# Kernel tuning notes

Measured on AMD Instinct MI355X. Metric: run time of the kernel, lower is better.

Reference implementation:

```python
import jax, jax.numpy as jnp
import numpy as np


def setup_inputs() -> dict:
    key = jax.random.key(0)
    B, U, I, H = 8192, 16, 128, 128
    k = jax.random.split(key, 6)
    s = 1.0 / np.sqrt(H)  # PyTorch GRU init scale (uniform(-s, s)); use scaled normal for test data
    return {
        "inputs": jax.random.normal(k[0], (B, U, I), dtype=jnp.float32),
        "hidden": jax.random.normal(k[1], (B, U, H), dtype=jnp.float32),
        "w_ih": jax.random.normal(k[2], (U, 3 * H, I), dtype=jnp.float32) * s,
        "w_hh": jax.random.normal(k[3], (U, 3 * H, H), dtype=jnp.float32) * s,
        "b_ih": jax.random.normal(k[4], (U, 3 * H), dtype=jnp.float32) * s,
        "b_hh": jax.random.normal(k[5], (U, 3 * H), dtype=jnp.float32) * s,
    }


def reference(inputs, hidden, w_ih, w_hh, b_ih, b_hh):
    # Grouped single-step GRU: one independent GRU cell per unit u, batched via einsum.
    # PyTorch GRU gate order in the 3H dim: [reset, update, new].
    H = hidden.shape[-1]
    # gates_x[b,u,g] = sum_i inputs[b,u,i] * w_ih[u,g,i] + b_ih[u,g]
    gx = jnp.einsum("bui,ugi->bug", inputs, w_ih) + b_ih  # (B, U, 3H)
    gh = jnp.einsum("buh,ugh->bug", hidden, w_hh) + b_hh  # (B, U, 3H)
    xr, xz, xn = gx[..., :H], gx[..., H:2 * H], gx[..., 2 * H:]
    hr, hz, hn = gh[..., :H], gh[..., H:2 * H], gh[..., 2 * H:]
    r = jax.nn.sigmoid(xr + hr)
    z = jax.nn.sigmoid(xz + hz)
    n = jnp.tanh(xn + r * hn)
    return (1.0 - z) * n + z * hidden  # (B, U, H)
```

## Files before the change

### kernel.cpp

```cpp
#include <hip/hip_runtime.h>
#include <hip/hip_bf16.h>

typedef __attribute__((ext_vector_type(8))) short  short8;
typedef __attribute__((ext_vector_type(4))) float  floatx4;

#define UH   2048
#define XPAD 264

#define MFMA16(a,b,c) __builtin_amdgcn_mfma_f32_16x16x32_bf16(a, b, c, 0, 0, 0)

static __device__ __forceinline__ unsigned int pkbf16(float a, float b) {
    __hip_bfloat162 p = __float22bfloat162_rn(make_float2(a, b));
    return *(unsigned int*)&p;
}

__global__ __launch_bounds__(256) void prep(const float* __restrict__ w_ih,
                                            const float* __restrict__ w_hh,
                                            const float* __restrict__ b_ih,
                                            const float* __restrict__ b_hh,
                                            __hip_bfloat16* __restrict__ Wc,
                                            float* __restrict__ bias_c) {
    if (blockIdx.x < 768) {
        int t   = blockIdx.x * 256 + threadIdx.x;
        int k8  = t & 31;
        int row = t >> 5;
        int u   = row / 384;
        int g   = row - u * 384;
        int k   = k8 * 8;
        const float* src = (k < 128) ? (w_ih + (size_t)row * 128 + k)
                                     : (w_hh + (size_t)row * 128 + (k - 128));
        float4 v0 = ((const float4*)src)[0];
        float4 v1 = ((const float4*)src)[1];
        uint4 w;
        w.x = pkbf16(v0.x, v0.y);
        w.y = pkbf16(v0.z, v0.w);
        w.z = pkbf16(v1.x, v1.y);
        w.w = pkbf16(v1.z, v1.w);
        int gt = g >> 4, lr = g & 15;
        int s  = k8 >> 2, lq = k8 & 3;
        size_t off = (size_t)((u * 24 + gt) * 8 + s) * 512 + (lq * 16 + lr) * 8;
        *(uint4*)(Wc + off) = w;
    } else {
        int idx = (blockIdx.x - 768) * 256 + threadIdx.x;
        int u = idx >> 9;
        int g = idx & 511;
        float v;
        if (g < 256)       v = b_ih[u * 384 + g] + b_hh[u * 384 + g];
        else if (g < 384)  v = b_ih[u * 384 + g];
        else               v = b_hh[u * 384 + (g - 128)];
        bias_c[idx] = v;
    }
}

__global__ __launch_bounds__(512, 2) void gru_fused(
    const float* __restrict__ inputs, const float* __restrict__ hidden,
    const __hip_bfloat16* __restrict__ Wc, const float* __restrict__ bias_c,
    float* __restrict__ out)
{
    __shared__ __align__(16) __hip_bfloat16 Xs[2][64][XPAD];

    const int bx   = blockIdx.x;
    const int u    = ((bx & 7) << 1) | ((bx >> 3) & 1);
    const int mt0  = (bx >> 4) * 8;
    const int tid  = threadIdx.x;
    const int lane = tid & 63;
    const int wv   = tid >> 6;
    const int lr   = lane & 15;
    const int lq   = lane >> 4;

    const short* WgU = (const short*)Wc + (size_t)u * 98304 + lane * 8;
    short8 fR[8], fZ[8], fN[8];
    #pragma unroll
    for (int s = 0; s < 8; ++s) {
        fR[s] = *(const short8*)(WgU + (size_t)(       wv * 8 + s) * 512);
        fZ[s] = *(const short8*)(WgU + (size_t)( 64 +  wv * 8 + s) * 512);
        fN[s] = *(const short8*)(WgU + (size_t)(128 +  wv * 8 + s) * 512);
    }

    const int   c   = wv * 16 + lr;
    const float br  = bias_c[u * 512 + c];
    const float bz  = bias_c[u * 512 + 128 + c];
    const float bxn = bias_c[u * 512 + 256 + c];
    const float bhn = bias_c[u * 512 + 384 + c];

    const int scol = (tid & 63) * 4;
    const float* sbase = ((scol < 128) ? (inputs + scol)
                                       : (hidden + (scol - 128)))
                       + (size_t)u * 128;

    float4 stg[8];

    auto ISSUE = [&](int mt) {
        const float* p = sbase + (size_t)(mt * 64 + wv) * UH;
        #pragma unroll
        for (int i = 0; i < 8; ++i)
            stg[i] = *(const float4*)(p + (size_t)(i * 8) * UH);
    };
    auto WRITE = [&](int buf) {
        #pragma unroll
        for (int i = 0; i < 8; ++i) {
            uint2 w;
            w.x = pkbf16(stg[i].x, stg[i].y);
            w.y = pkbf16(stg[i].z, stg[i].w);
            *(uint2*)&Xs[buf][i * 8 + wv][scol] = w;
        }
    };
    auto BARRIER = [&]() {
        asm volatile("s_waitcnt lgkmcnt(0)" ::: "memory");
        __builtin_amdgcn_sched_barrier(0);
        __builtin_amdgcn_s_barrier();
        __builtin_amdgcn_sched_barrier(0);
    };

    ISSUE(mt0 + 0);
    WRITE(0);
    ISSUE(mt0 + 1);
    BARRIER();

    #pragma unroll 1
    for (int j = 0; j < 8; ++j) {
        const int buf = j & 1;

        floatx4 aR[4], aZ[4], aXN[4], aHN[4];
        #pragma unroll
        for (int m4 = 0; m4 < 4; ++m4) {
            aR[m4]  = (floatx4){0.f, 0.f, 0.f, 0.f};
            aZ[m4]  = (floatx4){0.f, 0.f, 0.f, 0.f};
            aXN[m4] = (floatx4){0.f, 0.f, 0.f, 0.f};
            aHN[m4] = (floatx4){0.f, 0.f, 0.f, 0.f};
        }
        #pragma unroll
        for (int s = 0; s < 8; ++s) {
            short8 aF[4];
            #pragma unroll
            for (int m4 = 0; m4 < 4; ++m4)
                aF[m4] = *(const short8*)((const short*)&Xs[buf][m4 * 16 + lr][0]
                                          + s * 32 + lq * 8);
            #pragma unroll
            for (int m4 = 0; m4 < 4; ++m4) {
                aR[m4] = MFMA16(aF[m4], fR[s], aR[m4]);
                aZ[m4] = MFMA16(aF[m4], fZ[s], aZ[m4]);
                if (s < 4) aXN[m4] = MFMA16(aF[m4], fN[s], aXN[m4]);
                else       aHN[m4] = MFMA16(aF[m4], fN[s], aHN[m4]);
            }
        }

        float* obase = out + (size_t)(mt0 + j) * 64 * UH + u * 128 + c;
        #pragma unroll
        for (int m4 = 0; m4 < 4; ++m4) {
            #pragma unroll
            for (int r = 0; r < 4; ++r) {
                const int m = m4 * 16 + lq * 4 + r;
                float rv = __builtin_amdgcn_rcpf(1.f + __expf(-(aR[m4][r] + br)));
                float zv = __builtin_amdgcn_rcpf(1.f + __expf(-(aZ[m4][r] + bz)));
                float npre = (aXN[m4][r] + bxn) + rv * (aHN[m4][r] + bhn);
                float nv = 2.f * __builtin_amdgcn_rcpf(1.f + __expf(-2.f * npre)) - 1.f;
                float hv = __bfloat162float(Xs[buf][m][128 + c]);
                obase[(size_t)m * UH] = nv + zv * (hv - nv);
            }
        }

        if (j < 7) {
            WRITE(buf ^ 1);
            if (j < 6) ISSUE(mt0 + j + 2);
            BARRIER();
        }
    }
}


extern "C" void kernel_launch(void* const* d_in, const int* in_sizes, int n_in,
                              void* d_out, int out_size, void* d_ws, size_t ws_size,
                              hipStream_t stream) {
    const float* inputs = (const float*)d_in[0];
    const float* hidden = (const float*)d_in[1];
    const float* w_ih   = (const float*)d_in[2];
    const float* w_hh   = (const float*)d_in[3];
    const float* b_ih   = (const float*)d_in[4];
    const float* b_hh   = (const float*)d_in[5];
    float* out = (float*)d_out;

    __hip_bfloat16* Wc = (__hip_bfloat16*)d_ws;
    float* bias_c = (float*)((char*)d_ws + (size_t)16 * 384 * 256 * 2);

    prep<<<dim3(800), dim3(256), 0, stream>>>(w_ih, w_hh, b_ih, b_hh, Wc, bias_c);
    gru_fused<<<dim3(256), dim3(512), 0, stream>>>(inputs, hidden, Wc, bias_c, out);
}
```

Before: 200.3 us.

## Fuse weight conversion into GRU kernel and transpose MFMA for vectorized stores

Drops the separate prep kernel: each block loads fp32 weights directly, converts them to bf16 MFMA fragments in registers, and folds the biases into the accumulator initial values. The MFMA operand order is swapped so each lane holds four consecutive output columns, which allows float4 output stores and a vector read of h from LDS. The epilogue is moved after the next tile's LDS write and global issue, and the barrier is deferred to overlap it. This removes one launch and the workspace round trip. In exchange, each block redundantly converts its unit's weights, 16 blocks per unit.

```diff
diff --git a/kernel.cpp b/kernel.cpp
--- a/kernel.cpp
+++ b/kernel.cpp
@@ -13,48 +13,15 @@
     __hip_bfloat162 p = __float22bfloat162_rn(make_float2(a, b));
     return *(unsigned int*)&p;
 }
-
-__global__ __launch_bounds__(256) void prep(const float* __restrict__ w_ih,
-                                            const float* __restrict__ w_hh,
-                                            const float* __restrict__ b_ih,
-                                            const float* __restrict__ b_hh,
-                                            __hip_bfloat16* __restrict__ Wc,
-                                            float* __restrict__ bias_c) {
-    if (blockIdx.x < 768) {
-        int t   = blockIdx.x * 256 + threadIdx.x;
-        int k8  = t & 31;
-        int row = t >> 5;
-        int u   = row / 384;
-        int g   = row - u * 384;
-        int k   = k8 * 8;
-        const float* src = (k < 128) ? (w_ih + (size_t)row * 128 + k)
-                                     : (w_hh + (size_t)row * 128 + (k - 128));
-        float4 v0 = ((const float4*)src)[0];
-        float4 v1 = ((const float4*)src)[1];
-        uint4 w;
-        w.x = pkbf16(v0.x, v0.y);
-        w.y = pkbf16(v0.z, v0.w);
-        w.z = pkbf16(v1.x, v1.y);
-        w.w = pkbf16(v1.z, v1.w);
-        int gt = g >> 4, lr = g & 15;
-        int s  = k8 >> 2, lq = k8 & 3;
-        size_t off = (size_t)((u * 24 + gt) * 8 + s) * 512 + (lq * 16 + lr) * 8;
-        *(uint4*)(Wc + off) = w;
-    } else {
-        int idx = (blockIdx.x - 768) * 256 + threadIdx.x;
-        int u = idx >> 9;
-        int g = idx & 511;
-        float v;
-        if (g < 256)       v = b_ih[u * 384 + g] + b_hh[u * 384 + g];
-        else if (g < 384)  v = b_ih[u * 384 + g];
-        else               v = b_hh[u * 384 + (g - 128)];
-        bias_c[idx] = v;
-    }
+static __device__ __forceinline__ float bf2f(unsigned short h) {
+    unsigned int u = (unsigned int)h << 16;
+    return *(float*)&u;
 }
 
 __global__ __launch_bounds__(512, 2) void gru_fused(
     const float* __restrict__ inputs, const float* __restrict__ hidden,
-    const __hip_bfloat16* __restrict__ Wc, const float* __restrict__ bias_c,
+    const float* __restrict__ w_ih,   const float* __restrict__ w_hh,
+    const float* __restrict__ b_ih,   const float* __restrict__ b_hh,
     float* __restrict__ out)
 {
     __shared__ __align__(16) __hip_bfloat16 Xs[2][64][XPAD];
@@ -68,20 +35,40 @@
     const int lr   = lane & 15;
     const int lq   = lane >> 4;
 
-    const short* WgU = (const short*)Wc + (size_t)u * 98304 + lane * 8;
+    auto loadW = [&](int gt, int s) -> short8 {
+        const int row = gt * 16 + lr;
+        const int k0  = s * 32 + lq * 8;
+        const float* src = (k0 < 128)
+            ? (w_ih + (size_t)(u * 384 + row) * 128 + k0)
+            : (w_hh + (size_t)(u * 384 + row) * 128 + (k0 - 128));
+        float4 v0 = ((const float4*)src)[0];
+        float4 v1 = ((const float4*)src)[1];
+        union { uint4 q; short8 s8; } cvt;
+        cvt.q.x = pkbf16(v0.x, v0.y);
+        cvt.q.y = pkbf16(v0.z, v0.w);
+        cvt.q.z = pkbf16(v1.x, v1.y);
+        cvt.q.w = pkbf16(v1.z, v1.w);
+        return cvt.s8;
+    };
     short8 fR[8], fZ[8], fN[8];
     #pragma unroll
     for (int s = 0; s < 8; ++s) {
-        fR[s] = *(const short8*)(WgU + (size_t)(       wv * 8 + s) * 512);
-        fZ[s] = *(const short8*)(WgU + (size_t)( 64 +  wv * 8 + s) * 512);
-        fN[s] = *(const short8*)(WgU + (size_t)(128 +  wv * 8 + s) * 512);
+        fR[s] = loadW(     wv, s);
+        fZ[s] = loadW( 8 + wv, s);
+        fN[s] = loadW(16 + wv, s);
     }
 
-    const int   c   = wv * 16 + lr;
-    const float br  = bias_c[u * 512 + c];
-    const float bz  = bias_c[u * 512 + 128 + c];
-    const float bxn = bias_c[u * 512 + 256 + c];
-    const float bhn = bias_c[u * 512 + 384 + c];
+    const int c0 = wv * 16 + lq * 4;
+    float4 bi = *(const float4*)(b_ih + u * 384 +       c0);
+    float4 bh = *(const float4*)(b_hh + u * 384 +       c0);
+    float4 zi = *(const float4*)(b_ih + u * 384 + 128 + c0);
+    float4 zh = *(const float4*)(b_hh + u * 384 + 128 + c0);
+    float4 ni = *(const float4*)(b_ih + u * 384 + 256 + c0);
+    float4 nh = *(const float4*)(b_hh + u * 384 + 256 + c0);
+    const floatx4 accR0  = (floatx4){bi.x + bh.x, bi.y + bh.y, bi.z + bh.z, bi.w + bh.w};
+    const floatx4 accZ0  = (floatx4){zi.x + zh.x, zi.y + zh.y, zi.z + zh.z, zi.w + zh.w};
+    const floatx4 accXN0 = (floatx4){ni.x, ni.y, ni.z, ni.w};
+    const floatx4 accHN0 = (floatx4){nh.x, nh.y, nh.z, nh.w};
 
     const int scol = (tid & 63) * 4;
     const float* sbase = ((scol < 128) ? (inputs + scol)
@@ -113,6 +100,12 @@
     };
 
     ISSUE(mt0 + 0);
+    #pragma unroll
+    for (int s = 0; s < 8; ++s) {
+        asm volatile("" : "+v"(fR[s]));
+        asm volatile("" : "+v"(fZ[s]));
+        asm volatile("" : "+v"(fN[s]));
+    }
     WRITE(0);
     ISSUE(mt0 + 1);
     BARRIER();
@@ -124,47 +117,53 @@
         floatx4 aR[4], aZ[4], aXN[4], aHN[4];
         #pragma unroll
         for (int m4 = 0; m4 < 4; ++m4) {
-            aR[m4]  = (floatx4){0.f, 0.f, 0.f, 0.f};
-            aZ[m4]  = (floatx4){0.f, 0.f, 0.f, 0.f};
-            aXN[m4] = (floatx4){0.f, 0.f, 0.f, 0.f};
-            aHN[m4] = (floatx4){0.f, 0.f, 0.f, 0.f};
+            aR[m4]  = accR0;
+            aZ[m4]  = accZ0;
+            aXN[m4] = accXN0;
+            aHN[m4] = accHN0;
         }
         #pragma unroll
         for (int s = 0; s < 8; ++s) {
-            short8 aF[4];
+            short8 xF[4];
             #pragma unroll
             for (int m4 = 0; m4 < 4; ++m4)
-                aF[m4] = *(const short8*)((const short*)&Xs[buf][m4 * 16 + lr][0]
+                xF[m4] = *(const short8*)((const short*)&Xs[buf][m4 * 16 + lr][0]
                                           + s * 32 + lq * 8);
             #pragma unroll
             for (int m4 = 0; m4 < 4; ++m4) {
-                aR[m4] = MFMA16(aF[m4], fR[s], aR[m4]);
-                aZ[m4] = MFMA16(aF[m4], fZ[s], aZ[m4]);
-                if (s < 4) aXN[m4] = MFMA16(aF[m4], fN[s], aXN[m4]);
-                else       aHN[m4] = MFMA16(aF[m4], fN[s], aHN[m4]);
-            }
-        }
-
-        float* obase = out + (size_t)(mt0 + j) * 64 * UH + u * 128 + c;
-        #pragma unroll
-        for (int m4 = 0; m4 < 4; ++m4) {
-            #pragma unroll
-            for (int r = 0; r < 4; ++r) {
-                const int m = m4 * 16 + lq * 4 + r;
-                float rv = __builtin_amdgcn_rcpf(1.f + __expf(-(aR[m4][r] + br)));
-                float zv = __builtin_amdgcn_rcpf(1.f + __expf(-(aZ[m4][r] + bz)));
-                float npre = (aXN[m4][r] + bxn) + rv * (aHN[m4][r] + bhn);
-                float nv = 2.f * __builtin_amdgcn_rcpf(1.f + __expf(-2.f * npre)) - 1.f;
-                float hv = __bfloat162float(Xs[buf][m][128 + c]);
-                obase[(size_t)m * UH] = nv + zv * (hv - nv);
+                aR[m4] = MFMA16(fR[s], xF[m4], aR[m4]);
+                aZ[m4] = MFMA16(fZ[s], xF[m4], aZ[m4]);
+                if (s < 4) aXN[m4] = MFMA16(fN[s], xF[m4], aXN[m4]);
+                else       aHN[m4] = MFMA16(fN[s], xF[m4], aHN[m4]);
             }
         }
 
         if (j < 7) {
             WRITE(buf ^ 1);
             if (j < 6) ISSUE(mt0 + j + 2);
-            BARRIER();
         }
+
+        #pragma unroll
+        for (int m4 = 0; m4 < 4; ++m4) {
+            const int m = m4 * 16 + lr;
+            ushort4 hq = *(const ushort4*)&Xs[buf][m][128 + c0];
+            unsigned short hs[4] = {hq.x, hq.y, hq.z, hq.w};
+            float4 o;
+            float* op = (float*)&o;
+            #pragma unroll
+            for (int r = 0; r < 4; ++r) {
+                float rv = __builtin_amdgcn_rcpf(1.f + __expf(-aR[m4][r]));
+                float zv = __builtin_amdgcn_rcpf(1.f + __expf(-aZ[m4][r]));
+                float npre = aXN[m4][r] + rv * aHN[m4][r];
+                float nv = 2.f * __builtin_amdgcn_rcpf(1.f + __expf(-2.f * npre)) - 1.f;
+                float hv = bf2f(hs[r]);
+                op[r] = nv + zv * (hv - nv);
+            }
+            float* orow = out + (size_t)((mt0 + j) * 64 + m) * UH + u * 128 + c0;
+            *(float4*)orow = o;
+        }
+
+        if (j < 7) BARRIER();
     }
 }
 
@@ -180,9 +179,6 @@
     const float* b_hh   = (const float*)d_in[5];
     float* out = (float*)d_out;
 
-    __hip_bfloat16* Wc = (__hip_bfloat16*)d_ws;
-    float* bias_c = (float*)((char*)d_ws + (size_t)16 * 384 * 256 * 2);
-
-    prep<<<dim3(800), dim3(256), 0, stream>>>(w_ih, w_hh, b_ih, b_hh, Wc, bias_c);
-    gru_fused<<<dim3(256), dim3(512), 0, stream>>>(inputs, hidden, Wc, bias_c, out);
+    gru_fused<<<dim3(256), dim3(512), 0, stream>>>(inputs, hidden,
+                                                   w_ih, w_hh, b_ih, b_hh, out);
 }
```

After: 202.8 us. No clear change (+1.3%).

## Shrink batch tile, stream weights from global per step, swap MFMA operands for vector stores

Applied to the files above, without the earlier changes.

Each block now handles 128 batch rows in 32-row tiles instead of 512 in 64-row tiles, and the grid grows to 1024 blocks with launch bounds raised to 4 blocks per CU. Weight fragments are reloaded from global/L2 on every k-step instead of being held in registers. This frees registers for higher occupancy but adds repeated weight traffic. MFMA operands are swapped so each lane owns four contiguous output columns, which allows float4 stores and float4 fp32 hidden loads. Biases now initialize the accumulators, and the hidden term uses the exact fp32 value rather than the bf16 copy in LDS.

```diff
diff --git a/kernel.cpp b/kernel.cpp
--- a/kernel.cpp
+++ b/kernel.cpp
@@ -52,53 +52,43 @@
     }
 }
 
-__global__ __launch_bounds__(512, 2) void gru_fused(
+__global__ __launch_bounds__(512, 4) void gru_fused(
     const float* __restrict__ inputs, const float* __restrict__ hidden,
     const __hip_bfloat16* __restrict__ Wc, const float* __restrict__ bias_c,
     float* __restrict__ out)
 {
-    __shared__ __align__(16) __hip_bfloat16 Xs[2][64][XPAD];
+    __shared__ __align__(16) __hip_bfloat16 Xs[2][32][XPAD];
 
     const int bx   = blockIdx.x;
     const int u    = ((bx & 7) << 1) | ((bx >> 3) & 1);
-    const int mt0  = (bx >> 4) * 8;
+    const int r0   = (bx >> 4) * 128;
     const int tid  = threadIdx.x;
     const int lane = tid & 63;
     const int wv   = tid >> 6;
     const int lr   = lane & 15;
     const int lq   = lane >> 4;
 
-    const short* WgU = (const short*)Wc + (size_t)u * 98304 + lane * 8;
-    short8 fR[8], fZ[8], fN[8];
-    #pragma unroll
-    for (int s = 0; s < 8; ++s) {
-        fR[s] = *(const short8*)(WgU + (size_t)(       wv * 8 + s) * 512);
-        fZ[s] = *(const short8*)(WgU + (size_t)( 64 +  wv * 8 + s) * 512);
-        fN[s] = *(const short8*)(WgU + (size_t)(128 +  wv * 8 + s) * 512);
-    }
+    const int c0 = wv * 16 + lq * 4;
+    const floatx4 accR0  = *(const floatx4*)(bias_c + u * 512 +       c0);
+    const floatx4 accZ0  = *(const floatx4*)(bias_c + u * 512 + 128 + c0);
+    const floatx4 accXN0 = *(const floatx4*)(bias_c + u * 512 + 256 + c0);
+    const floatx4 accHN0 = *(const floatx4*)(bias_c + u * 512 + 384 + c0);
 
-    const int   c   = wv * 16 + lr;
-    const float br  = bias_c[u * 512 + c];
-    const float bz  = bias_c[u * 512 + 128 + c];
-    const float bxn = bias_c[u * 512 + 256 + c];
-    const float bhn = bias_c[u * 512 + 384 + c];
-
-    const int scol = (tid & 63) * 4;
+    const int scol = lane * 4;
     const float* sbase = ((scol < 128) ? (inputs + scol)
                                        : (hidden + (scol - 128)))
                        + (size_t)u * 128;
 
-    float4 stg[8];
+    float4 stg[4];
 
-    auto ISSUE = [&](int mt) {
-        const float* p = sbase + (size_t)(mt * 64 + wv) * UH;
+    auto ISSUE = [&](int rowbase) {
         #pragma unroll
-        for (int i = 0; i < 8; ++i)
-            stg[i] = *(const float4*)(p + (size_t)(i * 8) * UH);
+        for (int i = 0; i < 4; ++i)
+            stg[i] = *(const float4*)(sbase + (size_t)(rowbase + i * 8 + wv) * UH);
     };
     auto WRITE = [&](int buf) {
         #pragma unroll
-        for (int i = 0; i < 8; ++i) {
+        for (int i = 0; i < 4; ++i) {
             uint2 w;
             w.x = pkbf16(stg[i].x, stg[i].y);
             w.y = pkbf16(stg[i].z, stg[i].w);
@@ -112,58 +102,60 @@
         __builtin_amdgcn_sched_barrier(0);
     };
 
-    ISSUE(mt0 + 0);
+    const short* WgU = (const short*)Wc + (size_t)u * 98304 + lane * 8;
+
+    ISSUE(r0);
     WRITE(0);
-    ISSUE(mt0 + 1);
+    ISSUE(r0 + 32);
     BARRIER();
 
     #pragma unroll 1
-    for (int j = 0; j < 8; ++j) {
+    for (int j = 0; j < 4; ++j) {
         const int buf = j & 1;
 
-        floatx4 aR[4], aZ[4], aXN[4], aHN[4];
-        #pragma unroll
-        for (int m4 = 0; m4 < 4; ++m4) {
-            aR[m4]  = (floatx4){0.f, 0.f, 0.f, 0.f};
-            aZ[m4]  = (floatx4){0.f, 0.f, 0.f, 0.f};
-            aXN[m4] = (floatx4){0.f, 0.f, 0.f, 0.f};
-            aHN[m4] = (floatx4){0.f, 0.f, 0.f, 0.f};
-        }
+        floatx4 aR[2]  = {accR0,  accR0};
+        floatx4 aZ[2]  = {accZ0,  accZ0};
+        floatx4 aXN[2] = {accXN0, accXN0};
+        floatx4 aHN[2] = {accHN0, accHN0};
         #pragma unroll
         for (int s = 0; s < 8; ++s) {
-            short8 aF[4];
+            short8 bR = *(const short8*)(WgU + (size_t)(      wv * 8 + s) * 512);
+            short8 bZ = *(const short8*)(WgU + (size_t)( 64 + wv * 8 + s) * 512);
+            short8 bN = *(const short8*)(WgU + (size_t)(128 + wv * 8 + s) * 512);
             #pragma unroll
-            for (int m4 = 0; m4 < 4; ++m4)
-                aF[m4] = *(const short8*)((const short*)&Xs[buf][m4 * 16 + lr][0]
-                                          + s * 32 + lq * 8);
-            #pragma unroll
-            for (int m4 = 0; m4 < 4; ++m4) {
-                aR[m4] = MFMA16(aF[m4], fR[s], aR[m4]);
-                aZ[m4] = MFMA16(aF[m4], fZ[s], aZ[m4]);
-                if (s < 4) aXN[m4] = MFMA16(aF[m4], fN[s], aXN[m4]);
-                else       aHN[m4] = MFMA16(aF[m4], fN[s], aHN[m4]);
+            for (int m4 = 0; m4 < 2; ++m4) {
+                short8 xF = *(const short8*)((const short*)&Xs[buf][m4 * 16 + lr][0]
+                                             + s * 32 + lq * 8);
+                aR[m4] = MFMA16(bR, xF, aR[m4]);
+                aZ[m4] = MFMA16(bZ, xF, aZ[m4]);
+                if (s < 4) aXN[m4] = MFMA16(bN, xF, aXN[m4]);
+                else       aHN[m4] = MFMA16(bN, xF, aHN[m4]);
             }
         }
 
-        float* obase = out + (size_t)(mt0 + j) * 64 * UH + u * 128 + c;
+        if (j < 3) {
+            WRITE(buf ^ 1);
+            if (j < 2) ISSUE(r0 + (j + 2) * 32);
+            BARRIER();
+        }
+
+        const int rowb = r0 + j * 32;
         #pragma unroll
-        for (int m4 = 0; m4 < 4; ++m4) {
+        for (int m4 = 0; m4 < 2; ++m4) {
+            const int m = rowb + m4 * 16 + lr;
+            float4 hq = *(const float4*)(hidden + (size_t)m * UH + u * 128 + c0);
+            const float hs[4] = {hq.x, hq.y, hq.z, hq.w};
+            float4 o;
+            float* op = (float*)&o;
             #pragma unroll
             for (int r = 0; r < 4; ++r) {
-                const int m = m4 * 16 + lq * 4 + r;
-                float rv = __builtin_amdgcn_rcpf(1.f + __expf(-(aR[m4][r] + br)));
-                float zv = __builtin_amdgcn_rcpf(1.f + __expf(-(aZ[m4][r] + bz)));
-                float npre = (aXN[m4][r] + bxn) + rv * (aHN[m4][r] + bhn);
+                float rv = __builtin_amdgcn_rcpf(1.f + __expf(-aR[m4][r]));
+                float zv = __builtin_amdgcn_rcpf(1.f + __expf(-aZ[m4][r]));
+                float npre = aXN[m4][r] + rv * aHN[m4][r];
                 float nv = 2.f * __builtin_amdgcn_rcpf(1.f + __expf(-2.f * npre)) - 1.f;
-                float hv = __bfloat162float(Xs[buf][m][128 + c]);
-                obase[(size_t)m * UH] = nv + zv * (hv - nv);
+                op[r] = nv + zv * (hs[r] - nv);
             }
-        }
-
-        if (j < 7) {
-            WRITE(buf ^ 1);
-            if (j < 6) ISSUE(mt0 + j + 2);
-            BARRIER();
+            *(float4*)(out + (size_t)m * UH + u * 128 + c0) = o;
         }
     }
 }
@@ -184,5 +176,5 @@
     float* bias_c = (float*)((char*)d_ws + (size_t)16 * 384 * 256 * 2);
 
     prep<<<dim3(800), dim3(256), 0, stream>>>(w_ih, w_hh, b_ih, b_hh, Wc, bias_c);
-    gru_fused<<<dim3(256), dim3(512), 0, stream>>>(inputs, hidden, Wc, bias_c, out);
+    gru_fused<<<dim3(1024), dim3(512), 0, stream>>>(inputs, hidden, Wc, bias_c, out);
 }
```

Result: slower. 314.9 us (+57.2%).
